# Performance work log

Measured on AMD Instinct MI355X. Metric: run time of the kernel, lower is better.

The kernel has to match this reference:

```python
import jax, jax.numpy as jnp
import numpy as np

HEAD = 8
EMB = 512
D_K = EMB // HEAD


def setup_inputs() -> dict:
    key = jax.random.key(0)
    ks = jax.random.split(key, 12)
    B, S = 2, 2048
    scale = 1.0 / np.sqrt(EMB)
    inp = {
        "query": jax.random.normal(ks[0], (B, S, EMB), jnp.float32),
        "key": jax.random.normal(ks[1], (B, S, EMB), jnp.float32),
        "value": jax.random.normal(ks[2], (B, S, EMB), jnp.float32),
        # subsequentMask(size): lower-triangular causal mask, shape [1, S, S]
        "mask": jnp.tril(jnp.ones((1, S, S), jnp.int32)),
        "Wq": jax.random.normal(ks[3], (EMB, EMB), jnp.float32) * scale,
        "bq": jnp.zeros((EMB,), jnp.float32),
        "Wk": jax.random.normal(ks[4], (EMB, EMB), jnp.float32) * scale,
        "bk": jnp.zeros((EMB,), jnp.float32),
        "Wv": jax.random.normal(ks[5], (EMB, EMB), jnp.float32) * scale,
        "bv": jnp.zeros((EMB,), jnp.float32),
        "Wo": jax.random.normal(ks[6], (EMB, EMB), jnp.float32) * scale,
        "bo": jnp.zeros((EMB,), jnp.float32),
    }
    return inp


def _split_heads(x, B):
    # [B, S, E] -> [B, H, S, d_k]
    return x.reshape(B, -1, HEAD, D_K).transpose(0, 2, 1, 3)


def reference(query, key, value, mask, Wq, bq, Wk, bk, Wv, bv, Wo, bo):
    B, S, _ = query.shape
    # linear projections (x @ W^T + b, torch nn.Linear convention)
    q = _split_heads(query @ Wq.T + bq, B)
    k = _split_heads(key @ Wk.T + bk, B)
    v = _split_heads(value @ Wv.T + bv, B)
    # scaled dot-product attention; scores [B, H, S, S]
    scores = jnp.einsum('bhqd,bhkd->bhqk', q, k) / jnp.sqrt(jnp.float32(D_K))
    # mask [1,S,S] -> unsqueeze(0) -> [1,1,S,S]; masked_fill(mask==0, -1e9)
    m = mask[None, ...]  # [1, 1, S, S]
    scores = jnp.where(m == 0, jnp.float32(-1e9), scores)
    p_attn = jax.nn.softmax(scores, axis=-1)
    # dropout is identity at inference (deterministic reference)
    x = jnp.einsum('bhqk,bhkd->bhqd', p_attn, v)
    x = x.transpose(0, 2, 1, 3).reshape(B, S, EMB)
    return x @ Wo.T + bo
```

## Files before the change

kernel.cpp:

```cpp
#include <hip/hip_runtime.h>
#include <hip/hip_bf16.h>


#define SEQ 2048
#define EMB 512
#define NH  8
#define DKD 64

typedef __bf16 bf16x8 __attribute__((ext_vector_type(8)));
typedef ushort u16x8  __attribute__((ext_vector_type(8)));
typedef float  f32x4  __attribute__((ext_vector_type(4)));

__device__ __forceinline__ ushort f2bf(float f) {
  unsigned x = __float_as_uint(f);
  return (ushort)((x + 0x7fffu + ((x >> 16) & 1u)) >> 16);
}
__device__ __forceinline__ unsigned pkbf(float a, float b) {
  __hip_bfloat162 h = __float22bfloat162_rn(make_float2(a, b));
  unsigned u;
  __builtin_memcpy(&u, &h, 4);
  return u;
}

__device__ __forceinline__ void cp16(const ushort* g, ushort* l) {
  __builtin_amdgcn_global_load_lds(
      (const __attribute__((address_space(1))) void*)g,
      (__attribute__((address_space(3))) void*)l, 16, 0, 0);
}

__global__ __launch_bounds__(256) void cvt7(
    const float* s0, const float* s1, const float* s2, const float* s3,
    const float* s4, const float* s5, const float* s6,
    ushort* d0, ushort* d1, ushort* d2, ushort* d3,
    ushort* d4, ushort* d5, ushort* d6) {
  const float* src; ushort* dst; int n;
  switch (blockIdx.y) {
    case 0: src = s0; dst = d0; n = 2 * SEQ * EMB; break;
    case 1: src = s1; dst = d1; n = 2 * SEQ * EMB; break;
    case 2: src = s2; dst = d2; n = 2 * SEQ * EMB; break;
    case 3: src = s3; dst = d3; n = EMB * EMB;     break;
    case 4: src = s4; dst = d4; n = EMB * EMB;     break;
    case 5: src = s5; dst = d5; n = EMB * EMB;     break;
    default: src = s6; dst = d6; n = EMB * EMB;    break;
  }
  int i = (blockIdx.x * 256 + threadIdx.x) * 8;
  if (i >= n) return;
  float4 a = *reinterpret_cast<const float4*>(src + i);
  float4 b = *reinterpret_cast<const float4*>(src + i + 4);
  uint4 t = make_uint4(pkbf(a.x, a.y), pkbf(a.z, a.w),
                       pkbf(b.x, b.y), pkbf(b.z, b.w));
  *reinterpret_cast<uint4*>(dst + i) = t;
}

__device__ __forceinline__ void gemm_body(const ushort* __restrict__ X,
                                          const ushort* __restrict__ W,
                                          const float* __restrict__ bias,
                                          void* __restrict__ C,
                                          int mode, bool of32, float oscale,
                                          ushort* sA, ushort* sB) {
  const int N = EMB, K = EMB;
  const int tid = threadIdx.x;
  const int w = tid >> 6, lane = tid & 63, r16 = lane & 15, g = lane >> 4;
  const int nT = N / 64;
  const int m0 = (blockIdx.x / nT) * 128;
  const int n0 = (blockIdx.x % nT) * 64;
  const int wm = w * 32;

  f32x4 acc[2][4] = {};

  auto stage = [&](int buf, int k0) {
#pragma unroll
    for (int i = 0; i < 2; ++i) {
      const int s = i * 256 + w * 64 + lane;
      const int row = s >> 2;
      const int col = (s & 3) ^ ((row >> 1) & 3);
      cp16(X + (size_t)(m0 + row) * K + k0 + col * 8, sA + buf * 4096 + s * 8);
    }
    {
      const int s = w * 64 + lane;
      const int row = s >> 2;
      const int col = (s & 3) ^ ((row >> 1) & 3);
      cp16(W + (size_t)(n0 + row) * K + k0 + col * 8, sB + buf * 2048 + s * 8);
    }
  };

  stage(0, 0);
  const int NIT = K / 32;
  for (int it = 0; it < NIT; ++it) {
    const int cur = it & 1;
    __syncthreads();
    if (it + 1 < NIT) stage(cur ^ 1, (it + 1) * 32);

    const ushort* bA = sA + cur * 4096;
    const ushort* bB = sB + cur * 2048;
    bf16x8 af[2], bfr[4];
#pragma unroll
    for (int f = 0; f < 2; ++f) {
      const int row = wm + f * 16 + r16;
      af[f] = *reinterpret_cast<const bf16x8*>(bA + row * 32 + ((g ^ ((row >> 1) & 3)) << 3));
    }
#pragma unroll
    for (int t = 0; t < 4; ++t) {
      const int row = t * 16 + r16;
      bfr[t] = *reinterpret_cast<const bf16x8*>(bB + row * 32 + ((g ^ ((row >> 1) & 3)) << 3));
    }
#pragma unroll
    for (int f = 0; f < 2; ++f)
#pragma unroll
      for (int t = 0; t < 4; ++t)
        acc[f][t] = __builtin_amdgcn_mfma_f32_16x16x32_bf16(af[f], bfr[t], acc[f][t], 0, 0, 0);
  }

#pragma unroll
  for (int t = 0; t < 4; ++t) {
    const int n = n0 + t * 16 + r16;
    const float bv = bias[n];
#pragma unroll
    for (int f = 0; f < 2; ++f) {
#pragma unroll
      for (int r = 0; r < 4; ++r) {
        const int m = m0 + wm + f * 16 + g * 4 + r;
        const float v = (acc[f][t][r] + bv) * oscale;
        size_t addr;
        if (mode == 0) {
          addr = (size_t)m * N + n;
        } else {
          const int b = m >> 11, s = m & (SEQ - 1);
          const int h = n >> 6, dk = n & (DKD - 1);
          addr = (mode == 1) ? (((size_t)(b * NH + h) * SEQ + s) * DKD + dk)
                             : (((size_t)(b * NH + h) * DKD + dk) * SEQ + s);
        }
        if (of32) ((float*)C)[addr] = v;
        else      ((ushort*)C)[addr] = f2bf(v);
      }
    }
  }
}

__global__ __launch_bounds__(256) void proj_qkv(
    const ushort* Xq, const ushort* Xk, const ushort* Xv,
    const ushort* Wq, const ushort* Wk, const ushort* Wv,
    const float* bq, const float* bk, const float* bv,
    ushort* Qo, ushort* Ko, ushort* Vo) {
  __shared__ __align__(16) ushort sA[2 * 128 * 32];
  __shared__ __align__(16) ushort sB[2 * 64 * 32];
  const int z = blockIdx.z;
  const ushort* X = (z == 0) ? Xq : (z == 1) ? Xk : Xv;
  const ushort* W = (z == 0) ? Wq : (z == 1) ? Wk : Wv;
  const float* bias = (z == 0) ? bq : (z == 1) ? bk : bv;
  ushort* C = (z == 0) ? Qo : (z == 1) ? Ko : Vo;
  gemm_body(X, W, bias, C, (z == 2) ? 2 : 1, false,
            (z == 0) ? 0.18033688011112042f : 1.0f, sA, sB);
}

__global__ __launch_bounds__(256) void out_proj(const ushort* X, const ushort* W,
                                                const float* bias, float* C) {
  __shared__ __align__(16) ushort sA[2 * 128 * 32];
  __shared__ __align__(16) ushort sB[2 * 64 * 32];
  gemm_body(X, W, bias, C, 0, true, 1.0f, sA, sB);
}

__global__ __launch_bounds__(256) void flash_attn(const ushort* __restrict__ Q,
                                                  const ushort* __restrict__ Kb,
                                                  const ushort* __restrict__ Vt,
                                                  float* __restrict__ O0,
                                                  float* __restrict__ O1,
                                                  float* __restrict__ P0,
                                                  float* __restrict__ P1) {
  __shared__ __align__(16) ushort sK[2][64 * 64];
  __shared__ __align__(16) ushort sV[2][64 * 64];
  __shared__ __align__(16) ushort sP[4][16 * 64];

  const int tid = threadIdx.x, w = tid >> 6, lane = tid & 63;
  const int r16 = lane & 15, g = lane >> 4;
  const int g2 = blockIdx.x & 3;
  const int c  = blockIdx.x >> 2;
  const int bh = c & 15;
  const int t4 = c >> 4;
  const int qb = (g2 < 2) ? (31 - t4) : t4;
  const int half = g2 & 1;
  const int tiles = qb + 1;
  const int hs  = (tiles + 1) >> 1;
  const int kt0 = half ? hs : 0;
  const int kt1 = half ? tiles : hs;

  const int q0 = qb * 64 + w * 16;
  const int q  = q0 + r16;

  const ushort* qp = Q + ((size_t)bh * SEQ + q0 + r16) * DKD + g * 8;
  const bf16x8 qf0 = *reinterpret_cast<const bf16x8*>(qp);
  const bf16x8 qf1 = *reinterpret_cast<const bf16x8*>(qp + 32);

  f32x4 oacc[4] = {};
  float psum = 0.f;

  const ushort* kbase = Kb + (size_t)bh * SEQ * DKD;
  const ushort* vbase = Vt + (size_t)bh * DKD * SEQ;

  auto stageKV = [&](int buf, int kb) {
#pragma unroll
    for (int i = 0; i < 2; ++i) {
      const int s = i * 256 + w * 64 + lane;
      const int row = s >> 3;
      const int col = (s & 7) ^ (row & 7);
      cp16(kbase + (size_t)(kb + row) * DKD + col * 8, &sK[buf][(size_t)(i * 256 + w * 64) * 8]);
      cp16(vbase + (size_t)row * SEQ + kb + col * 8,   &sV[buf][(size_t)(i * 256 + w * 64) * 8]);
    }
  };

  if (kt0 < kt1) stageKV(0, kt0 * 64);
  for (int kt = kt0; kt < kt1; ++kt) {
    const int cur = (kt - kt0) & 1;
    const int kb = kt * 64;
    __syncthreads();
    if (kt + 1 < kt1) stageKV(cur ^ 1, (kt + 1) * 64);

    f32x4 sc[4] = {};
#pragma unroll
    for (int t = 0; t < 4; ++t) {
      const int row = t * 16 + r16;
      const bf16x8 a0 = *reinterpret_cast<const bf16x8*>(&sK[cur][row * 64 + (((0 + g) ^ (row & 7)) << 3)]);
      const bf16x8 a1 = *reinterpret_cast<const bf16x8*>(&sK[cur][row * 64 + (((4 + g) ^ (row & 7)) << 3)]);
      sc[t] = __builtin_amdgcn_mfma_f32_16x16x32_bf16(a0, qf0, sc[t], 0, 0, 0);
      sc[t] = __builtin_amdgcn_mfma_f32_16x16x32_bf16(a1, qf1, sc[t], 0, 0, 0);
    }

    const bool diag = (kb + 63) > q0;
    float p[16];
#pragma unroll
    for (int t = 0; t < 4; ++t)
#pragma unroll
      for (int r = 0; r < 4; ++r) {
        float e = __builtin_amdgcn_exp2f(sc[t][r]);
        if (diag && (kb + t * 16 + g * 4 + r) > q) e = 0.f;
        p[t * 4 + r] = e;
      }
    float s0 = (p[0] + p[1]) + (p[2] + p[3]);
    float s1 = (p[4] + p[5]) + (p[6] + p[7]);
    float s2 = (p[8] + p[9]) + (p[10] + p[11]);
    float s3 = (p[12] + p[13]) + (p[14] + p[15]);
    psum += (s0 + s1) + (s2 + s3);

#pragma unroll
    for (int t = 0; t < 4; ++t) {
      const unsigned lo = pkbf(p[t * 4],     p[t * 4 + 1]);
      const unsigned hi = pkbf(p[t * 4 + 2], p[t * 4 + 3]);
      const int key0 = t * 16 + g * 4;
      const int slot = (key0 >> 3) ^ (r16 & 7);
      *reinterpret_cast<uint2*>(&sP[w][r16 * 64 + slot * 8 + (key0 & 7)]) = make_uint2(lo, hi);
    }
    __asm__ volatile("s_waitcnt lgkmcnt(0)" ::: "memory");

    const bf16x8 pf0 = *reinterpret_cast<const bf16x8*>(&sP[w][r16 * 64 + (((0 + g) ^ (r16 & 7)) << 3)]);
    const bf16x8 pf1 = *reinterpret_cast<const bf16x8*>(&sP[w][r16 * 64 + (((4 + g) ^ (r16 & 7)) << 3)]);
#pragma unroll
    for (int t = 0; t < 4; ++t) {
      const int row = t * 16 + r16;
      const bf16x8 b0 = *reinterpret_cast<const bf16x8*>(&sV[cur][row * 64 + (((0 + g) ^ (row & 7)) << 3)]);
      const bf16x8 b1 = *reinterpret_cast<const bf16x8*>(&sV[cur][row * 64 + (((4 + g) ^ (row & 7)) << 3)]);
      oacc[t] = __builtin_amdgcn_mfma_f32_16x16x32_bf16(pf0, b0, oacc[t], 0, 0, 0);
      oacc[t] = __builtin_amdgcn_mfma_f32_16x16x32_bf16(pf1, b1, oacc[t], 0, 0, 0);
    }
  }

  psum += __shfl_xor(psum, 16);
  psum += __shfl_xor(psum, 32);
  float* Pc = half ? P1 : P0;
  float* Oc = half ? O1 : O0;
  if (g == 0) Pc[(size_t)bh * SEQ + q0 + r16] = psum;
#pragma unroll
  for (int r = 0; r < 4; ++r) {
    const int mq = q0 + g * 4 + r;
#pragma unroll
    for (int t = 0; t < 4; ++t)
      Oc[((size_t)bh * SEQ + mq) * DKD + t * 16 + r16] = oacc[t][r];
  }
}

__global__ __launch_bounds__(256) void attn_norm(const float* __restrict__ O0,
                                                 const float* __restrict__ O1,
                                                 const float* __restrict__ P0,
                                                 const float* __restrict__ P1,
                                                 ushort* __restrict__ Ab) {
  const int idx = blockIdx.x * 256 + threadIdx.x;
  const int d0 = (idx & 7) * 8;
  const int s  = (idx >> 3) & (SEQ - 1);
  const int bh = idx >> 14;
  const size_t o = ((size_t)bh * SEQ + s) * DKD + d0;
  const float4 a0 = *reinterpret_cast<const float4*>(O0 + o);
  const float4 a1 = *reinterpret_cast<const float4*>(O0 + o + 4);
  const float4 b0 = *reinterpret_cast<const float4*>(O1 + o);
  const float4 b1 = *reinterpret_cast<const float4*>(O1 + o + 4);
  const float inv = 1.0f / (P0[(size_t)bh * SEQ + s] + P1[(size_t)bh * SEQ + s]);
  uint4 t = make_uint4(
      pkbf((a0.x + b0.x) * inv, (a0.y + b0.y) * inv),
      pkbf((a0.z + b0.z) * inv, (a0.w + b0.w) * inv),
      pkbf((a1.x + b1.x) * inv, (a1.y + b1.y) * inv),
      pkbf((a1.z + b1.z) * inv, (a1.w + b1.w) * inv));
  const int b = bh >> 3, h = bh & 7;
  *reinterpret_cast<uint4*>(Ab + ((size_t)b * SEQ + s) * EMB + h * DKD + d0) = t;
}

extern "C" void kernel_launch(void* const* d_in, const int* in_sizes, int n_in,
                              void* d_out, int out_size, void* d_ws, size_t ws_size,
                              hipStream_t stream) {
  const float* q_in = (const float*)d_in[0];
  const float* k_in = (const float*)d_in[1];
  const float* v_in = (const float*)d_in[2];
  const float* Wq = (const float*)d_in[4];
  const float* bq = (const float*)d_in[5];
  const float* Wk = (const float*)d_in[6];
  const float* bk = (const float*)d_in[7];
  const float* Wv = (const float*)d_in[8];
  const float* bv = (const float*)d_in[9];
  const float* Wo = (const float*)d_in[10];
  const float* bo = (const float*)d_in[11];
  float* out = (float*)d_out;
  ushort* ws = (ushort*)d_ws;

  const size_t NX = (size_t)2 * SEQ * EMB;
  const size_t NW = (size_t)EMB * EMB;
  ushort* Xq = ws;
  ushort* Xk = Xq + NX;
  ushort* Xv = Xk + NX;
  ushort* WqB = Xv + NX;
  ushort* WkB = WqB + NW;
  ushort* WvB = WkB + NW;
  ushort* WoB = WvB + NW;
  ushort* Qb  = WoB + NW;
  ushort* Kbf = Qb + NX;
  ushort* Vbf = Kbf + NX;
  ushort* Ab  = Vbf + NX;
  float*  O0  = (float*)(Ab + NX);
  float*  O1  = O0 + (size_t)2 * NH * SEQ * DKD;
  float*  P0  = O1 + (size_t)2 * NH * SEQ * DKD;
  float*  P1  = P0 + (size_t)2 * NH * SEQ;

  dim3 blk(256);
  cvt7<<<dim3(1024, 7), blk, 0, stream>>>(q_in, k_in, v_in, Wq, Wk, Wv, Wo,
                                          Xq, Xk, Xv, WqB, WkB, WvB, WoB);
  proj_qkv<<<dim3((2 * SEQ / 128) * (EMB / 64), 1, 3), blk, 0, stream>>>(
      Xq, Xk, Xv, WqB, WkB, WvB, bq, bk, bv, Qb, Kbf, Vbf);
  flash_attn<<<dim3(16 * 32 * 2), blk, 0, stream>>>(Qb, Kbf, Vbf, O0, O1, P0, P1);
  attn_norm<<<dim3(1024), blk, 0, stream>>>(O0, O1, P0, P1, Ab);
  out_proj<<<dim3((2 * SEQ / 128) * (EMB / 64)), blk, 0, stream>>>(Ab, WoB, bo, out);
}
```

Measured before the change: 170.0 us.

## Fuse fp32-to-bf16 input conversion and attention normalization into GEMM A-tile staging

The GEMM A-operand staging now loads fp32 data directly and converts it to bf16 in registers before writing to LDS. The separate activation conversion pass and the attn_norm kernel are removed, and out_proj reads the split O0/O1/P0/P1 partials itself and normalizes them while staging. This cuts two kernel launches and the bf16 intermediate round trips through global memory. In exchange, each GEMM block re-reads fp32 A data (twice the bytes, plus redundant partial loads across N tiles), and the staging goes through synchronous register loads instead of async global-to-LDS copies, which can expose latency.

```diff
diff --git a/kernel.cpp b/kernel.cpp
--- a/kernel.cpp
+++ b/kernel.cpp
@@ -8,7 +8,6 @@
 #define DKD 64
 
 typedef __bf16 bf16x8 __attribute__((ext_vector_type(8)));
-typedef ushort u16x8  __attribute__((ext_vector_type(8)));
 typedef float  f32x4  __attribute__((ext_vector_type(4)));
 
 __device__ __forceinline__ ushort f2bf(float f) {
@@ -28,23 +27,17 @@
       (__attribute__((address_space(3))) void*)l, 16, 0, 0);
 }
 
-__global__ __launch_bounds__(256) void cvt7(
+__global__ __launch_bounds__(256) void cvtW(
     const float* s0, const float* s1, const float* s2, const float* s3,
-    const float* s4, const float* s5, const float* s6,
-    ushort* d0, ushort* d1, ushort* d2, ushort* d3,
-    ushort* d4, ushort* d5, ushort* d6) {
-  const float* src; ushort* dst; int n;
+    ushort* d0, ushort* d1, ushort* d2, ushort* d3) {
+  const float* src; ushort* dst;
   switch (blockIdx.y) {
-    case 0: src = s0; dst = d0; n = 2 * SEQ * EMB; break;
-    case 1: src = s1; dst = d1; n = 2 * SEQ * EMB; break;
-    case 2: src = s2; dst = d2; n = 2 * SEQ * EMB; break;
-    case 3: src = s3; dst = d3; n = EMB * EMB;     break;
-    case 4: src = s4; dst = d4; n = EMB * EMB;     break;
-    case 5: src = s5; dst = d5; n = EMB * EMB;     break;
-    default: src = s6; dst = d6; n = EMB * EMB;    break;
-  }
-  int i = (blockIdx.x * 256 + threadIdx.x) * 8;
-  if (i >= n) return;
+    case 0: src = s0; dst = d0; break;
+    case 1: src = s1; dst = d1; break;
+    case 2: src = s2; dst = d2; break;
+    default: src = s3; dst = d3; break;
+  }
+  const int i = (blockIdx.x * 256 + threadIdx.x) * 8;
   float4 a = *reinterpret_cast<const float4*>(src + i);
   float4 b = *reinterpret_cast<const float4*>(src + i + 4);
   uint4 t = make_uint4(pkbf(a.x, a.y), pkbf(a.z, a.w),
@@ -52,7 +45,12 @@
   *reinterpret_cast<uint4*>(dst + i) = t;
 }
 
-__device__ __forceinline__ void gemm_body(const ushort* __restrict__ X,
+template <int AMODE>
+__device__ __forceinline__ void gemm_body(const float* __restrict__ Xf,
+                                          const float* __restrict__ O0,
+                                          const float* __restrict__ O1,
+                                          const float* __restrict__ P0,
+                                          const float* __restrict__ P1,
                                           const ushort* __restrict__ W,
                                           const float* __restrict__ bias,
                                           void* __restrict__ C,
@@ -68,28 +66,54 @@
 
   f32x4 acc[2][4] = {};
 
-  auto stage = [&](int buf, int k0) {
+  auto stageA = [&](int buf, int k0) {
 #pragma unroll
     for (int i = 0; i < 2; ++i) {
       const int s = i * 256 + w * 64 + lane;
       const int row = s >> 2;
-      const int col = (s & 3) ^ ((row >> 1) & 3);
-      cp16(X + (size_t)(m0 + row) * K + k0 + col * 8, sA + buf * 4096 + s * 8);
-    }
-    {
-      const int s = w * 64 + lane;
-      const int row = s >> 2;
-      const int col = (s & 3) ^ ((row >> 1) & 3);
-      cp16(W + (size_t)(n0 + row) * K + k0 + col * 8, sB + buf * 2048 + s * 8);
+      const int c   = s & 3;
+      const int slot = c ^ ((row >> 1) & 3);
+      float4 x0, x1;
+      float scale = 1.0f;
+      if (AMODE == 1) {
+        const float* src = Xf + (size_t)(m0 + row) * K + k0 + c * 8;
+        x0 = *reinterpret_cast<const float4*>(src);
+        x1 = *reinterpret_cast<const float4*>(src + 4);
+      } else {
+        const int m = m0 + row;
+        const int b = m >> 11, ss = m & (SEQ - 1);
+        const int k = k0 + c * 8;
+        const int bh = b * NH + (k >> 6);
+        const size_t o = ((size_t)bh * SEQ + ss) * DKD + (k & (DKD - 1));
+        const float4 a0 = *reinterpret_cast<const float4*>(O0 + o);
+        const float4 a1 = *reinterpret_cast<const float4*>(O0 + o + 4);
+        const float4 b0 = *reinterpret_cast<const float4*>(O1 + o);
+        const float4 b1 = *reinterpret_cast<const float4*>(O1 + o + 4);
+        scale = 1.0f / (P0[(size_t)bh * SEQ + ss] + P1[(size_t)bh * SEQ + ss]);
+        x0 = make_float4(a0.x + b0.x, a0.y + b0.y, a0.z + b0.z, a0.w + b0.w);
+        x1 = make_float4(a1.x + b1.x, a1.y + b1.y, a1.z + b1.z, a1.w + b1.w);
+      }
+      uint4 t = make_uint4(pkbf(x0.x * scale, x0.y * scale),
+                           pkbf(x0.z * scale, x0.w * scale),
+                           pkbf(x1.x * scale, x1.y * scale),
+                           pkbf(x1.z * scale, x1.w * scale));
+      *reinterpret_cast<uint4*>(sA + buf * 4096 + row * 32 + slot * 8) = t;
     }
   };
-
-  stage(0, 0);
+  auto stageB = [&](int buf, int k0) {
+    const int s = w * 64 + lane;
+    const int row = s >> 2;
+    const int col = (s & 3) ^ ((row >> 1) & 3);
+    cp16(W + (size_t)(n0 + row) * K + k0 + col * 8, sB + buf * 2048 + s * 8);
+  };
+
+  stageA(0, 0);
+  stageB(0, 0);
   const int NIT = K / 32;
   for (int it = 0; it < NIT; ++it) {
     const int cur = it & 1;
     __syncthreads();
-    if (it + 1 < NIT) stage(cur ^ 1, (it + 1) * 32);
+    if (it + 1 < NIT) { stageB(cur ^ 1, (it + 1) * 32); stageA(cur ^ 1, (it + 1) * 32); }
 
     const ushort* bA = sA + cur * 4096;
     const ushort* bB = sB + cur * 2048;
@@ -138,26 +162,28 @@
 }
 
 __global__ __launch_bounds__(256) void proj_qkv(
-    const ushort* Xq, const ushort* Xk, const ushort* Xv,
+    const float* Xq, const float* Xk, const float* Xv,
     const ushort* Wq, const ushort* Wk, const ushort* Wv,
     const float* bq, const float* bk, const float* bv,
     ushort* Qo, ushort* Ko, ushort* Vo) {
   __shared__ __align__(16) ushort sA[2 * 128 * 32];
   __shared__ __align__(16) ushort sB[2 * 64 * 32];
   const int z = blockIdx.z;
-  const ushort* X = (z == 0) ? Xq : (z == 1) ? Xk : Xv;
+  const float* X = (z == 0) ? Xq : (z == 1) ? Xk : Xv;
   const ushort* W = (z == 0) ? Wq : (z == 1) ? Wk : Wv;
   const float* bias = (z == 0) ? bq : (z == 1) ? bk : bv;
   ushort* C = (z == 0) ? Qo : (z == 1) ? Ko : Vo;
-  gemm_body(X, W, bias, C, (z == 2) ? 2 : 1, false,
-            (z == 0) ? 0.18033688011112042f : 1.0f, sA, sB);
-}
-
-__global__ __launch_bounds__(256) void out_proj(const ushort* X, const ushort* W,
-                                                const float* bias, float* C) {
+  gemm_body<1>(X, nullptr, nullptr, nullptr, nullptr, W, bias, C,
+               (z == 2) ? 2 : 1, false,
+               (z == 0) ? 0.18033688011112042f : 1.0f, sA, sB);
+}
+
+__global__ __launch_bounds__(256) void out_proj(
+    const float* O0, const float* O1, const float* P0, const float* P1,
+    const ushort* W, const float* bias, float* C) {
   __shared__ __align__(16) ushort sA[2 * 128 * 32];
   __shared__ __align__(16) ushort sB[2 * 64 * 32];
-  gemm_body(X, W, bias, C, 0, true, 1.0f, sA, sB);
+  gemm_body<2>(nullptr, O0, O1, P0, P1, W, bias, C, 0, true, 1.0f, sA, sB);
 }
 
 __global__ __launch_bounds__(256) void flash_attn(const ushort* __restrict__ Q,
@@ -275,30 +301,6 @@
     for (int t = 0; t < 4; ++t)
       Oc[((size_t)bh * SEQ + mq) * DKD + t * 16 + r16] = oacc[t][r];
   }
-}
-
-__global__ __launch_bounds__(256) void attn_norm(const float* __restrict__ O0,
-                                                 const float* __restrict__ O1,
-                                                 const float* __restrict__ P0,
-                                                 const float* __restrict__ P1,
-                                                 ushort* __restrict__ Ab) {
-  const int idx = blockIdx.x * 256 + threadIdx.x;
-  const int d0 = (idx & 7) * 8;
-  const int s  = (idx >> 3) & (SEQ - 1);
-  const int bh = idx >> 14;
-  const size_t o = ((size_t)bh * SEQ + s) * DKD + d0;
-  const float4 a0 = *reinterpret_cast<const float4*>(O0 + o);
-  const float4 a1 = *reinterpret_cast<const float4*>(O0 + o + 4);
-  const float4 b0 = *reinterpret_cast<const float4*>(O1 + o);
-  const float4 b1 = *reinterpret_cast<const float4*>(O1 + o + 4);
-  const float inv = 1.0f / (P0[(size_t)bh * SEQ + s] + P1[(size_t)bh * SEQ + s]);
-  uint4 t = make_uint4(
-      pkbf((a0.x + b0.x) * inv, (a0.y + b0.y) * inv),
-      pkbf((a0.z + b0.z) * inv, (a0.w + b0.w) * inv),
-      pkbf((a1.x + b1.x) * inv, (a1.y + b1.y) * inv),
-      pkbf((a1.z + b1.z) * inv, (a1.w + b1.w) * inv));
-  const int b = bh >> 3, h = bh & 7;
-  *reinterpret_cast<uint4*>(Ab + ((size_t)b * SEQ + s) * EMB + h * DKD + d0) = t;
 }
 
 extern "C" void kernel_launch(void* const* d_in, const int* in_sizes, int n_in,
@@ -320,28 +322,23 @@
 
   const size_t NX = (size_t)2 * SEQ * EMB;
   const size_t NW = (size_t)EMB * EMB;
-  ushort* Xq = ws;
-  ushort* Xk = Xq + NX;
-  ushort* Xv = Xk + NX;
-  ushort* WqB = Xv + NX;
+  ushort* WqB = ws;
   ushort* WkB = WqB + NW;
   ushort* WvB = WkB + NW;
   ushort* WoB = WvB + NW;
   ushort* Qb  = WoB + NW;
   ushort* Kbf = Qb + NX;
   ushort* Vbf = Kbf + NX;
-  ushort* Ab  = Vbf + NX;
-  float*  O0  = (float*)(Ab + NX);
+  float*  O0  = (float*)(Vbf + NX);
   float*  O1  = O0 + (size_t)2 * NH * SEQ * DKD;
   float*  P0  = O1 + (size_t)2 * NH * SEQ * DKD;
   float*  P1  = P0 + (size_t)2 * NH * SEQ;
 
   dim3 blk(256);
-  cvt7<<<dim3(1024, 7), blk, 0, stream>>>(q_in, k_in, v_in, Wq, Wk, Wv, Wo,
-                                          Xq, Xk, Xv, WqB, WkB, WvB, WoB);
+  cvtW<<<dim3(128, 4), blk, 0, stream>>>(Wq, Wk, Wv, Wo, WqB, WkB, WvB, WoB);
   proj_qkv<<<dim3((2 * SEQ / 128) * (EMB / 64), 1, 3), blk, 0, stream>>>(
-      Xq, Xk, Xv, WqB, WkB, WvB, bq, bk, bv, Qb, Kbf, Vbf);
+      q_in, k_in, v_in, WqB, WkB, WvB, bq, bk, bv, Qb, Kbf, Vbf);
   flash_attn<<<dim3(16 * 32 * 2), blk, 0, stream>>>(Qb, Kbf, Vbf, O0, O1, P0, P1);
-  attn_norm<<<dim3(1024), blk, 0, stream>>>(O0, O1, P0, P1, Ab);
-  out_proj<<<dim3((2 * SEQ / 128) * (EMB / 64)), blk, 0, stream>>>(Ab, WoB, bo, out);
-}
+  out_proj<<<dim3((2 * SEQ / 128) * (EMB / 64)), blk, 0, stream>>>(
+      O0, O1, P0, P1, WoB, bo, out);
+}
```

After: 182.7 us. +7.5%, slower.
